# Kernel tuning notes

Measured on AMD Instinct MI355X. Metric: run time of the kernel, lower is better.

The kernel has to match this reference:

```python
import jax, jax.numpy as jnp
import numpy as np

N = 50000       # nodes per side (all node sets share N so concat along dim 1 works)
E = 500000      # edges per relation
B = 64          # graphs for global_mean_pool
C = 32          # per-layer hidden (latent_dim = (32,32) x10)
D = 288         # sum(latent_dim[1:,0]) = 9*32
NUM_CLASSES = 10
NUM_LAYERS = 9


def _tconv(x_s, x_d, ei, Wq, bq, Wk, bk, Wv, bv, Ws, bs, edge_feat=None, We=None):
    """PyG TransformerConv: heads=1, concat=True, beta=False, root_weight=True."""
    q = x_d @ Wq + bq                       # [Nd, C]
    k = x_s @ Wk + bk                       # [Ns, C]
    v = x_s @ Wv + bv                       # [Ns, C]
    src, dst = ei[0], ei[1]
    ke = k[src]                             # gather per edge [E, C]
    ve = v[src]
    if We is not None:                      # lin_edge (bias=False); added to key AND value
        e = edge_feat @ We
        ke = ke + e
        ve = ve + e
    nd = x_d.shape[0]
    logits = jnp.sum(q[dst] * ke, axis=-1) / jnp.sqrt(jnp.float32(C))
    m = jax.ops.segment_max(logits, dst, num_segments=nd)      # segment softmax
    ex = jnp.exp(logits - m[dst])
    denom = jax.ops.segment_sum(ex, dst, num_segments=nd)
    alpha = ex / (denom[dst] + 1e-16)
    agg = jax.ops.segment_sum(ve * alpha[:, None], dst, num_segments=nd)
    return agg + x_d @ Ws + bs              # root/skip linear (lin_skip)


def _forward(inter_emb, edge_attr, uv_target_emb,
             inter_index, uv_target_index, target_uv_index, batch,
             conv_Wq, conv_bq, conv_Wk, conv_bk, conv_Wv, conv_bv,
             conv_Ws, conv_bs, conv_We,
             lin_W1, lin_b1, lin_W2, lin_b2, lin_W3, lin_b3,
             lin_W4, lin_b4, lin_W5, lin_b5, lin_W6, lin_b6):
    f0, f1 = jnp.split(inter_emb, 2, axis=1)            # torch.chunk(x, 2, dim=1)
    edge_feat = jnp.tile(edge_attr[:, None], (1, C))    # at.reshape(-1,1).repeat(1,C)
    states = []
    x = None
    for i in range(NUM_LAYERS):
        p = (conv_Wq[i], conv_bq[i], conv_Wk[i], conv_bk[i],
             conv_Wv[i], conv_bv[i], conv_Ws[i], conv_bs[i])
        if i % 3 == 0:
            xs, xd = (f0, f1) if i == 0 else (x, x)
            x = jnp.tanh(_tconv(xs, xd, inter_index, *p, edge_feat, conv_We[i // 3]))
        elif i % 3 == 1:
            x = jnp.tanh(_tconv(x, uv_target_emb, uv_target_index, *p))
        else:
            x = jnp.tanh(_tconv(uv_target_emb, x, target_uv_index, *p))
        states.append(x)
    h = jnp.concatenate(states, axis=1) @ lin_W1 + lin_b1        # [N, 288]
    sums = jax.ops.segment_sum(h, batch, num_segments=B)
    cnt = jax.ops.segment_sum(jnp.ones((h.shape[0],), h.dtype), batch, num_segments=B)
    pooled = sums / jnp.maximum(cnt, 1.0)[:, None]               # global_mean_pool
    h = jax.nn.relu(pooled @ lin_W2 + lin_b2)
    h = h @ lin_W3 + lin_b3
    h = h @ lin_W4 + lin_b4
    h = h @ lin_W5 + lin_b5
    h = h @ lin_W6 + lin_b6
    return jax.nn.log_softmax(h, axis=-1)                        # [B, NUM_CLASSES]


def setup_inputs():
    key = jax.random.key(0)
    ks = iter(jax.random.split(key, 64))
    def nrm(shape, scale=1.0):
        return jax.random.normal(next(ks), shape, dtype=jnp.float32) * jnp.float32(scale)
    s = 1.0 / np.sqrt(C)
    inp = {
        "inter_emb": nrm((N, 2 * C)),
        "edge_attr": nrm((E,)),
        "uv_target_emb": nrm((N, C)),
        "inter_index": jax.random.randint(next(ks), (2, E), 0, N, dtype=jnp.int32),
        "uv_target_index": jax.random.randint(next(ks), (2, E), 0, N, dtype=jnp.int32),
        "target_uv_index": jax.random.randint(next(ks), (2, E), 0, N, dtype=jnp.int32),
        "batch": jnp.sort(jax.random.randint(next(ks), (N,), 0, B, dtype=jnp.int32)),
        "conv_Wq": nrm((NUM_LAYERS, C, C), s), "conv_bq": nrm((NUM_LAYERS, C), 0.01),
        "conv_Wk": nrm((NUM_LAYERS, C, C), s), "conv_bk": nrm((NUM_LAYERS, C), 0.01),
        "conv_Wv": nrm((NUM_LAYERS, C, C), s), "conv_bv": nrm((NUM_LAYERS, C), 0.01),
        "conv_Ws": nrm((NUM_LAYERS, C, C), s), "conv_bs": nrm((NUM_LAYERS, C), 0.01),
        "conv_We": nrm((3, C, C), s),
        "lin_W1": nrm((D, D), 1.0 / np.sqrt(D)), "lin_b1": nrm((D,), 0.01),
        "lin_W2": nrm((D, D // 2), 1.0 / np.sqrt(D)), "lin_b2": nrm((D // 2,), 0.01),
        "lin_W3": nrm((D // 2, D // 2), 1.0 / np.sqrt(D // 2)), "lin_b3": nrm((D // 2,), 0.01),
        "lin_W4": nrm((D // 2, D // 4), 1.0 / np.sqrt(D // 2)), "lin_b4": nrm((D // 4,), 0.01),
        "lin_W5": nrm((D // 4, D // 4), 1.0 / np.sqrt(D // 4)), "lin_b5": nrm((D // 4,), 0.01),
        "lin_W6": nrm((D // 4, NUM_CLASSES), 1.0 / np.sqrt(D // 4)), "lin_b6": nrm((NUM_CLASSES,), 0.01),
    }
    return inp


def reference(inter_emb, edge_attr, uv_target_emb,
              inter_index, uv_target_index, target_uv_index, batch,
              conv_Wq, conv_bq, conv_Wk, conv_bk, conv_Wv, conv_bv,
              conv_Ws, conv_bs, conv_We,
              lin_W1, lin_b1, lin_W2, lin_b2, lin_W3, lin_b3,
              lin_W4, lin_b4, lin_W5, lin_b5, lin_W6, lin_b6):
    return _forward(inter_emb, edge_attr, uv_target_emb,
                    inter_index, uv_target_index, target_uv_index, batch,
                    conv_Wq, conv_bq, conv_Wk, conv_bk, conv_Wv, conv_bv,
                    conv_Ws, conv_bs, conv_We,
                    lin_W1, lin_b1, lin_W2, lin_b2, lin_W3, lin_b3,
                    lin_W4, lin_b4, lin_W5, lin_b5, lin_W6, lin_b6)
```

## Files before the change

### kernel.cpp

```cpp
#include <hip/hip_runtime.h>
#include <hip/hip_fp16.h>
#include <math.h>

#define RSQRT32 0.17677669529663687f
#define NS 8
#define NC 32
#define MAXBS 6336
#define TILE 2048

typedef float fx2 __attribute__((ext_vector_type(2)));


__global__ void hist_lds(const int* __restrict__ e0, const int* __restrict__ e1,
                         const int* __restrict__ e2, int E, int N, int BS, int CH,
                         unsigned short* __restrict__ partial) {
    __shared__ unsigned int h[MAXBS];
    int blk = blockIdx.x;
    int c = blk % NC, s = (blk / NC) % NS, r = blk / (NC * NS);
    int lo = s * BS, hi = min(lo + BS, N), nb = hi - lo;
    for (int i = threadIdx.x; i < nb; i += 256) h[i] = 0;
    __syncthreads();
    const int* ei = (r == 0) ? e0 : ((r == 1) ? e1 : e2);
    int ebeg = c * CH, eend = min(ebeg + CH, E);
    const int* dst = ei + E;
    for (int i = ebeg + (int)threadIdx.x; i < eend; i += 256) {
        int d = dst[i];
        if (d >= lo && d < hi) atomicAdd(&h[d - lo], 1u);
    }
    __syncthreads();
    unsigned short* out = partial + ((size_t)blk) * BS;
    for (int i = threadIdx.x; i < nb; i += 256) out[i] = (unsigned short)h[i];
}

__global__ void chunk_scan(unsigned short* __restrict__ partial, int* __restrict__ cnt3,
                           int N, int BS) {
    int t = blockIdx.x * blockDim.x + threadIdx.x;
    int tot = 3 * NS * BS;
    if (t >= tot) return;
    int r = t / (NS * BS);
    int rem = t - r * NS * BS;
    int s = rem / BS, bin = rem - s * BS;
    int d = s * BS + bin;
    if (d >= N) return;
    size_t base = ((size_t)(r * NS + s) * NC) * BS + bin;
    unsigned int run = 0;
    for (int c = 0; c < NC; ++c) {
        unsigned int v = partial[base + (size_t)c * BS];
        partial[base + (size_t)c * BS] = (unsigned short)run;
        run += v;
    }
    cnt3[(size_t)r * N + d] = (int)run;
}

__global__ void scan_tiles_sum(const int* __restrict__ cnt3, int* __restrict__ tsum,
                               int N, int G) {
    int blk = blockIdx.x, r = blk / G, g = blk - r * G;
    int base = g * TILE;
    const int* cnt = cnt3 + (size_t)r * N;
    int s = 0;
    for (int i = threadIdx.x; i < TILE; i += 256) {
        int idx = base + i;
        s += (idx < N) ? cnt[idx] : 0;
    }
    __shared__ int wsum[4];
    for (int m = 32; m; m >>= 1) s += __shfl_down(s, m);
    if ((threadIdx.x & 63) == 0) wsum[threadIdx.x >> 6] = s;
    __syncthreads();
    if (threadIdx.x == 0) tsum[blk] = wsum[0] + wsum[1] + wsum[2] + wsum[3];
}

__global__ void scan_offsets(int* __restrict__ tsum, int* __restrict__ rp3, int N, int G) {
    int r = threadIdx.x;
    if (r < 3) {
        int run = 0;
        for (int g = 0; g < G; ++g) { int v = tsum[r * G + g]; tsum[r * G + g] = run; run += v; }
        rp3[(size_t)r * (N + 1) + N] = run;
    }
}

__global__ void scan_write(const int* __restrict__ cnt3, const int* __restrict__ toff,
                           int* __restrict__ rp3, int N, int G) {
    int blk = blockIdx.x, r = blk / G, g = blk - r * G;
    int base = g * TILE;
    const int* cnt = cnt3 + (size_t)r * N;
    int* rp = rp3 + (size_t)r * (N + 1);
    __shared__ int part[256];
    int t = threadIdx.x;
    int v[8]; int s = 0;
    #pragma unroll
    for (int j = 0; j < 8; ++j) {
        int idx = base + t * 8 + j;
        int x = (idx < N) ? cnt[idx] : 0;
        v[j] = s; s += x;
    }
    part[t] = s;
    __syncthreads();
    for (int off = 1; off < 256; off <<= 1) {
        int x = (t >= off) ? part[t - off] : 0;
        __syncthreads();
        part[t] += x;
        __syncthreads();
    }
    int texcl = part[t] - s + toff[blk];
    #pragma unroll
    for (int j = 0; j < 8; ++j) {
        int idx = base + t * 8 + j;
        if (idx < N) rp[idx] = texcl + v[j];
    }
}

__global__ void scatter_cs(const int* __restrict__ e0, const int* __restrict__ e1,
                           const int* __restrict__ e2, const float* __restrict__ ea,
                           const unsigned short* __restrict__ partial,
                           const int* __restrict__ rp3,
                           int2* __restrict__ adj0, int* __restrict__ adj12,
                           int E, int N, int BS, int CH) {
    __shared__ unsigned int cur[MAXBS];
    int blk = blockIdx.x;
    int s = blk & 7;
    int rest = blk >> 3;
    int c = rest % NC, r = rest / NC;
    int pblk = c + NC * (s + NS * r);
    int lo = s * BS, hi = min(lo + BS, N), nb = hi - lo;
    const unsigned short* po = partial + ((size_t)pblk) * BS;
    const int* rp = rp3 + (size_t)r * (N + 1);
    for (int i = threadIdx.x; i < nb; i += 256)
        cur[i] = (unsigned int)rp[lo + i] + (unsigned int)po[i];
    __syncthreads();
    const int* ei = (r == 0) ? e0 : ((r == 1) ? e1 : e2);
    const int* srcp = ei;
    const int* dstp = ei + E;
    int ebeg = c * CH, eend = min(ebeg + CH, E);
    if (r == 0) {
        for (int i = ebeg + (int)threadIdx.x; i < eend; i += 256) {
            int d = dstp[i];
            if (d < lo || d >= hi) continue;
            unsigned int pos = atomicAdd(&cur[d - lo], 1u);
            int2 v; v.x = srcp[i]; v.y = __float_as_int(ea[i]);
            adj0[pos] = v;
        }
    } else {
        int* adj = adj12 + (size_t)(r - 1) * E;
        for (int i = ebeg + (int)threadIdx.x; i < eend; i += 256) {
            int d = dstp[i];
            if (d < lo || d >= hi) continue;
            unsigned int pos = atomicAdd(&cur[d - lo], 1u);
            adj[pos] = srcp[i];
        }
    }
}


__global__ void colsum_kernel(const float* __restrict__ We, float* __restrict__ u,
                              int* __restrict__ bstart, int* __restrict__ bend, int B) {
    int t = threadIdx.x;
    if (t < 96) {
        int w = t >> 5, j = t & 31;
        const float* W = We + w * 1024;
        float s = 0.f;
        #pragma unroll
        for (int kk = 0; kk < 32; ++kk) s += W[kk * 32 + j];
        u[t] = s;
    }
    if (t < B) { bstart[t] = 0; bend[t] = 0; }
}

__global__ void bounds_kernel(const int* __restrict__ batch, int* __restrict__ bstart,
                              int* __restrict__ bend, int N) {
    int t = blockIdx.x * blockDim.x + threadIdx.x;
    if (t >= N) return;
    int b = batch[t];
    if (t == 0 || batch[t - 1] != b) bstart[b] = t;
    if (t == N - 1 || batch[t + 1] != b) bend[b] = t + 1;
}

__global__ void qkvs_kernel(
    const float* __restrict__ xs, int ssrc,
    const float* __restrict__ xd, int sdst,
    const float* __restrict__ Wq, const float* __restrict__ bq,
    const float* __restrict__ Wk, const float* __restrict__ bk,
    const float* __restrict__ Wv, const float* __restrict__ bv,
    const float* __restrict__ Ws, const float* __restrict__ bs,
    const float* __restrict__ u,
    float* __restrict__ qb, uint2* __restrict__ kv8,
    float* __restrict__ sb, float* __restrict__ qdu, int N)
{
    int lane = threadIdx.x & 63;
    int wid  = __builtin_amdgcn_readfirstlane((int)(threadIdx.x >> 6));
    int wpb  = blockDim.x >> 6;
    int gw   = blockIdx.x * wpb + wid;
    int nw   = gridDim.x * wpb;
    int j    = lane & 31;
    bool lower = lane < 32;

    const float* W1 = lower ? Wq : Wk;
    const float* W2 = lower ? Wv : Ws;
    float rw1[32], rw2[32];
    #pragma unroll
    for (int kk = 0; kk < 32; ++kk) {
        rw1[kk] = W1[kk * 32 + j];
        rw2[kk] = W2[kk * 32 + j];
    }
    float bias1 = lower ? bq[j] : bk[j];
    float bias2 = lower ? bv[j] : bs[j];
    float uj = (u != nullptr) ? u[j] : 0.f;

    for (int n = gw; n < N; n += nw) {
        const float* xdr = xd + (size_t)n * sdst;
        const float* xsr = xs + (size_t)n * ssrc;
        float acc1 = bias1, acc2 = bias2;
        #pragma unroll
        for (int kk = 0; kk < 32; ++kk) {
            float xdv = xdr[kk];
            float xsv = xsr[kk];
            float a  = lower ? xdv : xsv;
            float bb = lower ? xsv : xdv;
            acc1 = fmaf(a,  rw1[kk], acc1);
            acc2 = fmaf(bb, rw2[kk], acc2);
        }
        float kk_ = __shfl(acc1, j + 32);
        float k1 = __shfl_down(kk_, 1), v1 = __shfl_down(acc2, 1);
        float k2 = __shfl_down(kk_, 2), v2 = __shfl_down(acc2, 2);
        float k3 = __shfl_down(kk_, 3), v3 = __shfl_down(acc2, 3);
        if (lower) {
            qb[(size_t)n * 32 + j] = acc1;
            if ((j & 3) == 0) {
                int pk = __builtin_amdgcn_cvt_pk_fp8_f32(kk_, k1, 0, false);
                pk = __builtin_amdgcn_cvt_pk_fp8_f32(k2, k3, pk, true);
                int pv = __builtin_amdgcn_cvt_pk_fp8_f32(acc2, v1, 0, false);
                pv = __builtin_amdgcn_cvt_pk_fp8_f32(v2, v3, pv, true);
                kv8[(size_t)n * 8 + (j >> 2)] = make_uint2((unsigned)pk, (unsigned)pv);
            }
        } else {
            sb[(size_t)n * 32 + j] = acc2;
        }
        if (u != nullptr) {
            float pp = lower ? acc1 * uj : 0.f;
            pp += __shfl_xor(pp, 16);
            pp += __shfl_xor(pp, 8);
            pp += __shfl_xor(pp, 4);
            pp += __shfl_xor(pp, 2);
            pp += __shfl_xor(pp, 1);
            if (lane == 0) qdu[n] = pp * RSQRT32;
        }
    }
}

template<int HAS_EA>
__global__ __launch_bounds__(256, 8)
void agg_kernel(const int* __restrict__ rp, const void* __restrict__ adjv,
    const float* __restrict__ qb, const uint2* __restrict__ kv8,
    const float* __restrict__ qdu, const float* __restrict__ u,
    const float* __restrict__ skp, float* __restrict__ xout, int N)
{
    int t = threadIdx.x;
    int lane = t & 63;
    int cq = lane & 7;
    int o  = lane >> 3;
    int wv = t >> 6;
    int n = (blockIdx.x * 4 + wv) * 8 + o;
    if (n >= N) return;
    float4 qc = ((const float4*)(qb + (size_t)n * 32))[cq];
    float qd = HAS_EA ? qdu[n] : 0.f;
    float4 uc = HAS_EA ? ((const float4*)u)[cq] : make_float4(0.f, 0.f, 0.f, 0.f);
    int beg = rp[n], end = rp[n + 1];
    const int2* adjE = (const int2*)adjv;
    const int*  adjP = (const int*)adjv;
    float den0 = 0.f, den1 = 0.f;
    float4 num0 = make_float4(0.f, 0.f, 0.f, 0.f);
    float4 num1 = make_float4(0.f, 0.f, 0.f, 0.f);
    int i = beg;
    for (; i + 1 < end; i += 2) {
        int s0, s1; float ae0 = 0.f, ae1 = 0.f;
        if (HAS_EA) {
            int2 a0 = adjE[i], a1 = adjE[i + 1];
            s0 = a0.x; s1 = a1.x;
            ae0 = __int_as_float(a0.y); ae1 = __int_as_float(a1.y);
        } else { s0 = adjP[i]; s1 = adjP[i + 1]; }
        uint2 p0 = kv8[(size_t)s0 * 8 + cq];
        uint2 p1 = kv8[(size_t)s1 * 8 + cq];
        fx2 k001 = __builtin_amdgcn_cvt_pk_f32_fp8((int)p0.x, false);
        fx2 k023 = __builtin_amdgcn_cvt_pk_f32_fp8((int)p0.x, true);
        fx2 w001 = __builtin_amdgcn_cvt_pk_f32_fp8((int)p0.y, false);
        fx2 w023 = __builtin_amdgcn_cvt_pk_f32_fp8((int)p0.y, true);
        fx2 k101 = __builtin_amdgcn_cvt_pk_f32_fp8((int)p1.x, false);
        fx2 k123 = __builtin_amdgcn_cvt_pk_f32_fp8((int)p1.x, true);
        fx2 w101 = __builtin_amdgcn_cvt_pk_f32_fp8((int)p1.y, false);
        fx2 w123 = __builtin_amdgcn_cvt_pk_f32_fp8((int)p1.y, true);
        float d0 = fmaf(qc.x, k001[0], fmaf(qc.y, k001[1], fmaf(qc.z, k023[0], qc.w * k023[1])));
        float d1 = fmaf(qc.x, k101[0], fmaf(qc.y, k101[1], fmaf(qc.z, k123[0], qc.w * k123[1])));
        d0 += __shfl_xor(d0, 1);  d1 += __shfl_xor(d1, 1);
        d0 += __shfl_xor(d0, 2);  d1 += __shfl_xor(d1, 2);
        d0 += __shfl_xor(d0, 4);  d1 += __shfl_xor(d1, 4);
        float ex0 = __expf(fmaf(ae0, qd, d0 * RSQRT32));
        float ex1 = __expf(fmaf(ae1, qd, d1 * RSQRT32));
        den0 += ex0;  den1 += ex1;
        num0.x = fmaf(fmaf(ae0, uc.x, w001[0]), ex0, num0.x);
        num0.y = fmaf(fmaf(ae0, uc.y, w001[1]), ex0, num0.y);
        num0.z = fmaf(fmaf(ae0, uc.z, w023[0]), ex0, num0.z);
        num0.w = fmaf(fmaf(ae0, uc.w, w023[1]), ex0, num0.w);
        num1.x = fmaf(fmaf(ae1, uc.x, w101[0]), ex1, num1.x);
        num1.y = fmaf(fmaf(ae1, uc.y, w101[1]), ex1, num1.y);
        num1.z = fmaf(fmaf(ae1, uc.z, w123[0]), ex1, num1.z);
        num1.w = fmaf(fmaf(ae1, uc.w, w123[1]), ex1, num1.w);
    }
    if (i < end) {
        int s0; float ae0 = 0.f;
        if (HAS_EA) { int2 a0 = adjE[i]; s0 = a0.x; ae0 = __int_as_float(a0.y); }
        else s0 = adjP[i];
        uint2 p0 = kv8[(size_t)s0 * 8 + cq];
        fx2 k001 = __builtin_amdgcn_cvt_pk_f32_fp8((int)p0.x, false);
        fx2 k023 = __builtin_amdgcn_cvt_pk_f32_fp8((int)p0.x, true);
        fx2 w001 = __builtin_amdgcn_cvt_pk_f32_fp8((int)p0.y, false);
        fx2 w023 = __builtin_amdgcn_cvt_pk_f32_fp8((int)p0.y, true);
        float d0 = fmaf(qc.x, k001[0], fmaf(qc.y, k001[1], fmaf(qc.z, k023[0], qc.w * k023[1])));
        d0 += __shfl_xor(d0, 1);
        d0 += __shfl_xor(d0, 2);
        d0 += __shfl_xor(d0, 4);
        float ex0 = __expf(fmaf(ae0, qd, d0 * RSQRT32));
        den0 += ex0;
        num0.x = fmaf(fmaf(ae0, uc.x, w001[0]), ex0, num0.x);
        num0.y = fmaf(fmaf(ae0, uc.y, w001[1]), ex0, num0.y);
        num0.z = fmaf(fmaf(ae0, uc.z, w023[0]), ex0, num0.z);
        num0.w = fmaf(fmaf(ae0, uc.w, w023[1]), ex0, num0.w);
    }
    float den = den0 + den1;
    float inv = 1.f / (den + 1e-16f);
    float4 sk = ((const float4*)(skp + (size_t)n * 32))[cq];
    float4 ov;
    ov.x = tanhf(fmaf(num0.x + num1.x, inv, sk.x));
    ov.y = tanhf(fmaf(num0.y + num1.y, inv, sk.y));
    ov.z = tanhf(fmaf(num0.z + num1.z, inv, sk.z));
    ov.w = tanhf(fmaf(num0.w + num1.w, inv, sk.w));
    ((float4*)(xout + (size_t)n * 32))[cq] = ov;
}

__global__ void pool_kernel(const float* __restrict__ x,
                            const int* __restrict__ bstart, const int* __restrict__ bend,
                            float* __restrict__ poolsum, int layer_off) {
    __shared__ float red[256];
    int b = blockIdx.x >> 3, sub = blockIdx.x & 7;
    int s0 = bstart[b], s1 = bend[b];
    int cnt = s1 - s0;
    int n0 = s0 + (int)((long long)cnt * sub / 8);
    int n1 = s0 + (int)((long long)cnt * (sub + 1) / 8);
    int t = threadIdx.x, col = t & 31, g = t >> 5;
    float acc = 0.f;
    for (int n = n0 + g; n < n1; n += 8)
        acc += x[(size_t)n * 32 + col];
    red[t] = acc;
    __syncthreads();
    if (t < 32) {
        float s = red[t];
        #pragma unroll
        for (int k = 1; k < 8; ++k) s += red[t + 32 * k];
        atomicAdd(&poolsum[(size_t)b * 288 + layer_off + t], s);
    }
}


__device__ __forceinline__ void gemv_step(const float* __restrict__ W, const float* __restrict__ bias,
    const float* sin_, float* sout, int K, int M, int t, bool do_relu) {
    if (t < M) {
        float acc = bias[t];
        for (int kk = 0; kk < K; ++kk) acc = fmaf(sin_[kk], W[kk * M + t], acc);
        sout[t] = do_relu ? fmaxf(acc, 0.f) : acc;
    }
    __syncthreads();
}

__global__ void head_kernel(const float* __restrict__ poolsum,
    const int* __restrict__ bstart, const int* __restrict__ bend,
    const float* __restrict__ W1, const float* __restrict__ b1,
    const float* __restrict__ W2, const float* __restrict__ b2,
    const float* __restrict__ W3, const float* __restrict__ b3,
    const float* __restrict__ W4, const float* __restrict__ b4,
    const float* __restrict__ W5, const float* __restrict__ b5,
    const float* __restrict__ W6, const float* __restrict__ b6,
    float* __restrict__ out)
{
    __shared__ float ha[288], hb[288];
    __shared__ float lse;
    int b = blockIdx.x, t = threadIdx.x;
    float invc = 1.f / fmaxf((float)(bend[b] - bstart[b]), 1.f);
    if (t < 288) ha[t] = poolsum[(size_t)b * 288 + t] * invc;
    __syncthreads();
    gemv_step(W1, b1, ha, hb, 288, 288, t, false);
    gemv_step(W2, b2, hb, ha, 288, 144, t, true);
    gemv_step(W3, b3, ha, hb, 144, 144, t, false);
    gemv_step(W4, b4, hb, ha, 144, 72,  t, false);
    gemv_step(W5, b5, ha, hb, 72,  72,  t, false);
    gemv_step(W6, b6, hb, ha, 72,  10,  t, false);
    if (t == 0) {
        float m = ha[0];
        for (int i = 1; i < 10; ++i) m = fmaxf(m, ha[i]);
        float ssum = 0.f;
        for (int i = 0; i < 10; ++i) ssum += __expf(ha[i] - m);
        lse = m + logf(ssum);
    }
    __syncthreads();
    if (t < 10) out[b * 10 + t] = ha[t] - lse;
}


extern "C" void kernel_launch(void* const* d_in, const int* in_sizes, int n_in,
                              void* d_out, int out_size, void* d_ws, size_t ws_size,
                              hipStream_t stream)
{
    const float* inter_emb = (const float*)d_in[0];
    const float* edge_attr = (const float*)d_in[1];
    const float* uv_emb    = (const float*)d_in[2];
    const int* inter_idx = (const int*)d_in[3];
    const int* uvt_idx   = (const int*)d_in[4];
    const int* tuv_idx   = (const int*)d_in[5];
    const int* batch     = (const int*)d_in[6];
    const float* cWq = (const float*)d_in[7];  const float* cbq = (const float*)d_in[8];
    const float* cWk = (const float*)d_in[9];  const float* cbk = (const float*)d_in[10];
    const float* cWv = (const float*)d_in[11]; const float* cbv = (const float*)d_in[12];
    const float* cWs = (const float*)d_in[13]; const float* cbs = (const float*)d_in[14];
    const float* cWe = (const float*)d_in[15];
    const float* W1 = (const float*)d_in[16]; const float* b1 = (const float*)d_in[17];
    const float* W2 = (const float*)d_in[18]; const float* b2 = (const float*)d_in[19];
    const float* W3 = (const float*)d_in[20]; const float* b3 = (const float*)d_in[21];
    const float* W4 = (const float*)d_in[22]; const float* b4 = (const float*)d_in[23];
    const float* W5 = (const float*)d_in[24]; const float* b5 = (const float*)d_in[25];
    const float* W6 = (const float*)d_in[26]; const float* b6 = (const float*)d_in[27];

    const int N = in_sizes[2] / 32;
    const int E = in_sizes[1];
    const int B = out_size / 10;
    const int G = (N + TILE - 1) / TILE;
    const int BS = (N + NS - 1) / NS;
    const int CH = (E + NC - 1) / NC;

    char* p = (char*)d_ws;
    auto alloc = [&](size_t bytes) { char* r = p; p += (bytes + 255) & ~(size_t)255; return r; };
    float*   qb    = (float*)alloc((size_t)N * 32 * 4);
    uint2*   kv8   = (uint2*)alloc((size_t)N * 64);
    float*   sb    = (float*)alloc((size_t)N * 32 * 4);
    float*   qdu   = (float*)alloc((size_t)N * 4);
    float*   xa    = (float*)alloc((size_t)N * 32 * 4);
    float*   xb    = (float*)alloc((size_t)N * 32 * 4);
    float*   ub    = (float*)alloc(96 * 4);
    float*   poolsum = (float*)alloc((size_t)B * 288 * 4);
    int*     bstart = (int*)alloc((size_t)B * 4);
    int*     bend   = (int*)alloc((size_t)B * 4);
    int*     cnt3  = (int*)alloc((size_t)3 * N * 4);
    int*     rp3   = (int*)alloc((size_t)3 * (N + 1) * 4);
    int*     tsum  = (int*)alloc((size_t)3 * G * 4);
    unsigned short* partial = (unsigned short*)alloc((size_t)3 * NS * NC * BS * 2);
    int2*    adj0  = (int2*)alloc((size_t)E * 8);
    int*     adj12 = (int*)alloc((size_t)2 * E * 4);

    hist_lds<<<3 * NS * NC, 256, 0, stream>>>(inter_idx, uvt_idx, tuv_idx, E, N, BS, CH, partial);
    chunk_scan<<<(3 * NS * BS + 255) / 256, 256, 0, stream>>>(partial, cnt3, N, BS);
    scan_tiles_sum<<<3 * G, 256, 0, stream>>>(cnt3, tsum, N, G);
    scan_offsets<<<1, 64, 0, stream>>>(tsum, rp3, N, G);
    scan_write<<<3 * G, 256, 0, stream>>>(cnt3, tsum, rp3, N, G);
    scatter_cs<<<3 * NS * NC, 256, 0, stream>>>(inter_idx, uvt_idx, tuv_idx, edge_attr,
                                                partial, rp3, adj0, adj12, E, N, BS, CH);

    hipMemsetAsync(poolsum, 0, (size_t)B * 288 * 4, stream);
    colsum_kernel<<<1, 128, 0, stream>>>(cWe, ub, bstart, bend, B);
    bounds_kernel<<<(N + 255) / 256, 256, 0, stream>>>(batch, bstart, bend, N);

    float* xcur = nullptr;
    float* xnext = xa;
    for (int i = 0; i < 9; ++i) {
        int r = i % 3;
        const float* xsrc; int ssrc; const float* xdst; int sdst;
        if (i == 0)      { xsrc = inter_emb; ssrc = 64; xdst = inter_emb + 32; sdst = 64; }
        else if (r == 0) { xsrc = xcur; ssrc = 32; xdst = xcur;  sdst = 32; }
        else if (r == 1) { xsrc = xcur; ssrc = 32; xdst = uv_emb; sdst = 32; }
        else             { xsrc = uv_emb; ssrc = 32; xdst = xcur; sdst = 32; }
        const float* ul = (r == 0) ? (ub + (i / 3) * 32) : nullptr;

        qkvs_kernel<<<1024, 256, 0, stream>>>(xsrc, ssrc, xdst, sdst,
            cWq + i * 1024, cbq + i * 32, cWk + i * 1024, cbk + i * 32,
            cWv + i * 1024, cbv + i * 32, cWs + i * 1024, cbs + i * 32,
            ul, qb, kv8, sb, qdu, N);
        const int* rpl = rp3 + (size_t)r * (N + 1);
        if (r == 0) {
            agg_kernel<1><<<(N + 31) / 32, 256, 0, stream>>>(
                rpl, adj0, qb, kv8, qdu, ul, sb, xnext, N);
        } else {
            agg_kernel<0><<<(N + 31) / 32, 256, 0, stream>>>(
                rpl, adj12 + (size_t)(r - 1) * E, qb, kv8, qdu, ul, sb, xnext, N);
        }
        pool_kernel<<<B * 8, 256, 0, stream>>>(xnext, bstart, bend, poolsum, i * 32);
        xcur = xnext;
        xnext = (xnext == xa) ? xb : xa;
    }

    head_kernel<<<B, 320, 0, stream>>>(poolsum, bstart, bend,
        W1, b1, W2, b2, W3, b3, W4, b4, W5, b5, W6, b6, (float*)d_out);
}
```

Baseline: 537.9 us.

## Sort destination nodes by in-degree to balance aggregation wavefronts

Adds a per-relation counting sort of destination nodes by in-degree (capped at 63) and has the aggregation kernel process nodes in that order through a permutation array. Nodes with similar degrees then share a wavefront, which is meant to cut lane divergence from uneven edge loops. The cost is three extra setup kernels, including a serial single-thread-per-relation scan, plus one indirect load per node. Reads and writes of q, skip and output rows become scattered instead of contiguous. The qkvs kernel also picks its row pointers once outside the loop instead of selecting per element.

```diff
diff --git a/kernel.cpp b/kernel.cpp
--- a/kernel.cpp
+++ b/kernel.cpp
@@ -7,6 +7,8 @@
 #define NC 32
 #define MAXBS 6336
 #define TILE 2048
+#define DCH 4096
+#define NDB 64
 
 typedef float fx2 __attribute__((ext_vector_type(2)));
 
@@ -147,6 +149,48 @@
             unsigned int pos = atomicAdd(&cur[d - lo], 1u);
             adj[pos] = srcp[i];
         }
+    }
+}
+
+
+__global__ void deg_hist(const int* __restrict__ cnt3, int* __restrict__ dpart,
+                         int N, int DG) {
+    __shared__ int h[NDB];
+    int blk = blockIdx.x, r = blk / DG, g = blk - r * DG;
+    if (threadIdx.x < NDB) h[threadIdx.x] = 0;
+    __syncthreads();
+    int base = g * DCH, endd = min(base + DCH, N);
+    for (int d = base + (int)threadIdx.x; d < endd; d += 256) {
+        int deg = min(cnt3[(size_t)r * N + d], NDB - 1);
+        atomicAdd(&h[deg], 1);
+    }
+    __syncthreads();
+    if (threadIdx.x < NDB) dpart[(size_t)blk * NDB + threadIdx.x] = h[threadIdx.x];
+}
+
+__global__ void deg_scan(int* __restrict__ dpart, int DG) {
+    int r = threadIdx.x;
+    if (r >= 3) return;
+    int run = 0;
+    for (int b = 0; b < NDB; ++b)
+        for (int g = 0; g < DG; ++g) {
+            size_t idx = ((size_t)(r * DG + g)) * NDB + b;
+            int v = dpart[idx]; dpart[idx] = run; run += v;
+        }
+}
+
+__global__ void deg_scatter(const int* __restrict__ cnt3, const int* __restrict__ dpart,
+                            int* __restrict__ perm3, int N, int DG) {
+    __shared__ int cur[NDB];
+    int blk = blockIdx.x, r = blk / DG, g = blk - r * DG;
+    if (threadIdx.x < NDB) cur[threadIdx.x] = dpart[(size_t)blk * NDB + threadIdx.x];
+    __syncthreads();
+    int base = g * DCH, endd = min(base + DCH, N);
+    int* perm = perm3 + (size_t)r * N;
+    for (int d = base + (int)threadIdx.x; d < endd; d += 256) {
+        int deg = min(cnt3[(size_t)r * N + d], NDB - 1);
+        int pos = atomicAdd(&cur[deg], 1);
+        perm[pos] = d;
     }
 }
 
@@ -195,6 +239,8 @@
 
     const float* W1 = lower ? Wq : Wk;
     const float* W2 = lower ? Wv : Ws;
+    const float* xp1 = lower ? xd : xs;  int st1 = lower ? sdst : ssrc;
+    const float* xp2 = lower ? xs : xd;  int st2 = lower ? ssrc : sdst;
     float rw1[32], rw2[32];
     #pragma unroll
     for (int kk = 0; kk < 32; ++kk) {
@@ -206,17 +252,13 @@
     float uj = (u != nullptr) ? u[j] : 0.f;
 
     for (int n = gw; n < N; n += nw) {
-        const float* xdr = xd + (size_t)n * sdst;
-        const float* xsr = xs + (size_t)n * ssrc;
+        const float* r1 = xp1 + (size_t)n * st1;
+        const float* r2 = xp2 + (size_t)n * st2;
         float acc1 = bias1, acc2 = bias2;
         #pragma unroll
         for (int kk = 0; kk < 32; ++kk) {
-            float xdv = xdr[kk];
-            float xsv = xsr[kk];
-            float a  = lower ? xdv : xsv;
-            float bb = lower ? xsv : xdv;
-            acc1 = fmaf(a,  rw1[kk], acc1);
-            acc2 = fmaf(bb, rw2[kk], acc2);
+            acc1 = fmaf(r1[kk], rw1[kk], acc1);
+            acc2 = fmaf(r2[kk], rw2[kk], acc2);
         }
         float kk_ = __shfl(acc1, j + 32);
         float k1 = __shfl_down(kk_, 1), v1 = __shfl_down(acc2, 1);
@@ -249,6 +291,7 @@
 template<int HAS_EA>
 __global__ __launch_bounds__(256, 8)
 void agg_kernel(const int* __restrict__ rp, const void* __restrict__ adjv,
+    const int* __restrict__ perm,
     const float* __restrict__ qb, const uint2* __restrict__ kv8,
     const float* __restrict__ qdu, const float* __restrict__ u,
     const float* __restrict__ skp, float* __restrict__ xout, int N)
@@ -258,8 +301,9 @@
     int cq = lane & 7;
     int o  = lane >> 3;
     int wv = t >> 6;
-    int n = (blockIdx.x * 4 + wv) * 8 + o;
-    if (n >= N) return;
+    int slot = (blockIdx.x * 4 + wv) * 8 + o;
+    if (slot >= N) return;
+    int n = perm[slot];
     float4 qc = ((const float4*)(qb + (size_t)n * 32))[cq];
     float qd = HAS_EA ? qdu[n] : 0.f;
     float4 uc = HAS_EA ? ((const float4*)u)[cq] : make_float4(0.f, 0.f, 0.f, 0.f);
@@ -432,6 +476,7 @@
     const int G = (N + TILE - 1) / TILE;
     const int BS = (N + NS - 1) / NS;
     const int CH = (E + NC - 1) / NC;
+    const int DG = (N + DCH - 1) / DCH;
 
     char* p = (char*)d_ws;
     auto alloc = [&](size_t bytes) { char* r = p; p += (bytes + 255) & ~(size_t)255; return r; };
@@ -448,6 +493,8 @@
     int*     cnt3  = (int*)alloc((size_t)3 * N * 4);
     int*     rp3   = (int*)alloc((size_t)3 * (N + 1) * 4);
     int*     tsum  = (int*)alloc((size_t)3 * G * 4);
+    int*     perm3 = (int*)alloc((size_t)3 * N * 4);
+    int*     dpart = (int*)alloc((size_t)3 * DG * NDB * 4);
     unsigned short* partial = (unsigned short*)alloc((size_t)3 * NS * NC * BS * 2);
     int2*    adj0  = (int2*)alloc((size_t)E * 8);
     int*     adj12 = (int*)alloc((size_t)2 * E * 4);
@@ -459,6 +506,10 @@
     scan_write<<<3 * G, 256, 0, stream>>>(cnt3, tsum, rp3, N, G);
     scatter_cs<<<3 * NS * NC, 256, 0, stream>>>(inter_idx, uvt_idx, tuv_idx, edge_attr,
                                                 partial, rp3, adj0, adj12, E, N, BS, CH);
+
+    deg_hist<<<3 * DG, 256, 0, stream>>>(cnt3, dpart, N, DG);
+    deg_scan<<<1, 64, 0, stream>>>(dpart, DG);
+    deg_scatter<<<3 * DG, 256, 0, stream>>>(cnt3, dpart, perm3, N, DG);
 
     hipMemsetAsync(poolsum, 0, (size_t)B * 288 * 4, stream);
     colsum_kernel<<<1, 128, 0, stream>>>(cWe, ub, bstart, bend, B);
@@ -480,12 +531,13 @@
             cWv + i * 1024, cbv + i * 32, cWs + i * 1024, cbs + i * 32,
             ul, qb, kv8, sb, qdu, N);
         const int* rpl = rp3 + (size_t)r * (N + 1);
+        const int* pml = perm3 + (size_t)r * N;
         if (r == 0) {
             agg_kernel<1><<<(N + 31) / 32, 256, 0, stream>>>(
-                rpl, adj0, qb, kv8, qdu, ul, sb, xnext, N);
+                rpl, adj0, pml, qb, kv8, qdu, ul, sb, xnext, N);
         } else {
             agg_kernel<0><<<(N + 31) / 32, 256, 0, stream>>>(
-                rpl, adj12 + (size_t)(r - 1) * E, qb, kv8, qdu, ul, sb, xnext, N);
+                rpl, adj12 + (size_t)(r - 1) * E, pml, qb, kv8, qdu, ul, sb, xnext, N);
         }
         pool_kernel<<<B * 8, 256, 0, stream>>>(xnext, bstart, bend, poolsum, i * 32);
         xcur = xnext;
```

Result: slower. 705.4 us (+31.1%).
